# Optimization experiments

Hardware: AMD Instinct MI355X
Metric: run time of the kernel (lower is better)

## Reference

```python
import jax, jax.numpy as jnp
import numpy as np

DIM = 1024
FF = 4096
E = 8
K = 2


def setup_inputs() -> dict:
    key = jax.random.key(0)
    ks = jax.random.split(key, 6)
    x = jax.random.normal(ks[0], (4, 2048, DIM), dtype=jnp.float32)
    wr = jax.random.normal(ks[1], (E, DIM), dtype=jnp.float32) * 0.02   # router weight [E, D]
    w1 = jax.random.normal(ks[2], (E, DIM, 2 * FF), dtype=jnp.float32) * 0.02  # SwiGLU in-proj
    b1 = jax.random.normal(ks[3], (E, 2 * FF), dtype=jnp.float32) * 0.02
    w2 = jax.random.normal(ks[4], (E, FF, DIM), dtype=jnp.float32) * 0.02  # SwiGLU out-proj
    b2 = jax.random.normal(ks[5], (E, DIM), dtype=jnp.float32) * 0.02
    return {"x": x, "wr": wr, "w1": w1, "b1": b1, "w2": w2, "b2": b2}


def reference(x, wr, w1, b1, w2, b2):
    B, T, D = x.shape
    n_experts = wr.shape[0]
    xf = x.reshape(B * T, D)                      # [N, D]
    logits = xf @ wr.T                            # [N, E]
    topk_vals, topk_idx = jax.lax.top_k(logits, K)  # [N, K]
    gates = jax.nn.softmax(topk_vals, axis=-1)      # [N, K]
    out = jnp.zeros_like(xf)
    for e in range(n_experts):
        # combined gate weight for tokens routed to expert e (0 otherwise)
        g_e = jnp.sum(jnp.where(topk_idx == e, gates, 0.0), axis=-1)  # [N]
        u = xf @ w1[e] + b1[e]                    # [N, 2F]
        a, b = jnp.split(u, 2, axis=-1)
        h = jax.nn.silu(a) * b                    # SwiGLU
        y_e = h @ w2[e] + b2[e]                   # [N, D]
        out = out + g_e[:, None] * y_e
    return out.reshape(B, T, D)
```

## Files before the change

kernel.cpp:

```cpp
#include <hip/hip_runtime.h>

#define NE 8
#define NTOK 8192
#define NDIM 1024
#define NFF 4096

typedef short bf16x8 __attribute__((ext_vector_type(8)));
typedef float f32x4 __attribute__((ext_vector_type(4)));
typedef unsigned short us_t;
typedef us_t us4 __attribute__((ext_vector_type(4)));

#define MFMA16 __builtin_amdgcn_mfma_f32_16x16x32_bf16

__device__ __forceinline__ us_t f2bf(float f) {
  unsigned int u = __float_as_uint(f);
  u += 0x7fffu + ((u >> 16) & 1u);
  return (us_t)(u >> 16);
}

__device__ __forceinline__ void gload16(const void* g, void* l) {
  __builtin_amdgcn_global_load_lds(
      (const __attribute__((address_space(1))) void*)g,
      (__attribute__((address_space(3))) void*)l, 16, 0, 0);
}

__global__ __launch_bounds__(256) void router_kernel(
    const float* __restrict__ x, const float* __restrict__ wr,
    int* __restrict__ counts, int* __restrict__ tok_list,
    int4* __restrict__ tok4, float2* __restrict__ gate2,
    us_t* __restrict__ xbf)
{
  __shared__ float wr_s[NE * NDIM];
  int tid = threadIdx.x;
#pragma unroll
  for (int i = 0; i < 8; ++i)
    ((float4*)wr_s)[tid + 256 * i] = ((const float4*)wr)[tid + 256 * i];
  __syncthreads();
  int w = tid >> 6, l = tid & 63;
  int t = blockIdx.x * 4 + w;
  float4 xv[4];
#pragma unroll
  for (int j = 0; j < 4; ++j) xv[j] = ((const float4*)x)[(size_t)t * 256 + j * 64 + l];
#pragma unroll
  for (int j = 0; j < 4; ++j) {
    us4 o;
    o.x = f2bf(xv[j].x); o.y = f2bf(xv[j].y); o.z = f2bf(xv[j].z); o.w = f2bf(xv[j].w);
    ((us4*)xbf)[(size_t)t * 256 + j * 64 + l] = o;
  }
  float logits[NE];
#pragma unroll
  for (int e = 0; e < NE; ++e) {
    float p = 0.f;
#pragma unroll
    for (int j = 0; j < 4; ++j) {
      float4 wv = ((const float4*)wr_s)[e * 256 + j * 64 + l];
      p += xv[j].x * wv.x + xv[j].y * wv.y + xv[j].z * wv.z + xv[j].w * wv.w;
    }
#pragma unroll
    for (int s = 32; s > 0; s >>= 1) p += __shfl_xor(p, s, 64);
    logits[e] = p;
  }
  if (l == 0) {
    int e1 = 0; float v1 = logits[0];
#pragma unroll
    for (int e = 1; e < NE; ++e) if (logits[e] > v1) { v1 = logits[e]; e1 = e; }
    int e2 = -1; float v2 = -3.4e38f;
#pragma unroll
    for (int e = 0; e < NE; ++e) if (e != e1 && logits[e] > v2) { v2 = logits[e]; e2 = e; }
    float ge = expf(v2 - v1);
    float g1 = 1.f / (1.f + ge);
    float g2 = 1.f - g1;
    int i1 = atomicAdd(&counts[e1], 1);
    tok_list[e1 * NTOK + i1] = t;
    int i2 = atomicAdd(&counts[e2], 1);
    tok_list[e2 * NTOK + i2] = t;
    tok4[t] = make_int4(e1, i1, e2, i2);
    gate2[t] = make_float2(g1, g2);
  }
}

__global__ void prefix8(const int* __restrict__ counts, int* __restrict__ offsets) {
  if (threadIdx.x == 0) {
    int s = 0;
    for (int e = 0; e < NE; ++e) { offsets[e] = s; s += counts[e]; }
  }
}

__global__ __launch_bounds__(256) void transpose_cvt(
    const float* __restrict__ in, us_t* __restrict__ out, int R, int C)
{
  __shared__ float tile[64][65];
  int e = blockIdx.z;
  const float* ip = in + (size_t)e * R * C;
  us_t* op = out + (size_t)e * R * C;
  int r0 = blockIdx.y * 64, c0 = blockIdx.x * 64;
  int tid = threadIdx.x;
#pragma unroll
  for (int q = 0; q < 4; ++q) {
    int id = tid + 256 * q;
    int rr = id >> 4, c4 = id & 15;
    float4 v = *(const float4*)&ip[(size_t)(r0 + rr) * C + c0 + c4 * 4];
    tile[rr][c4 * 4 + 0] = v.x; tile[rr][c4 * 4 + 1] = v.y;
    tile[rr][c4 * 4 + 2] = v.z; tile[rr][c4 * 4 + 3] = v.w;
  }
  __syncthreads();
#pragma unroll
  for (int q = 0; q < 4; ++q) {
    int id = tid + 256 * q;
    int cc = id >> 4, r4 = id & 15;
    us4 o;
    o.x = f2bf(tile[r4 * 4 + 0][cc]);
    o.y = f2bf(tile[r4 * 4 + 1][cc]);
    o.z = f2bf(tile[r4 * 4 + 2][cc]);
    o.w = f2bf(tile[r4 * 4 + 3][cc]);
    *(us4*)&op[(size_t)(c0 + cc) * R + r0 + r4 * 4] = o;
  }
}

__global__ __launch_bounds__(256) void gemm1_swiglu(
    const us_t* __restrict__ xbf,
    const us_t* __restrict__ w1T,
    const float* __restrict__ b1,
    const int* __restrict__ counts, const int* __restrict__ offsets,
    const int* __restrict__ tok_list,
    us_t* __restrict__ hbuf)
{
  const int e = blockIdx.z, mt = blockIdx.y, ct = blockIdx.x;
  const int cnt = counts[e];
  if (mt * 128 >= cnt) return;
  const int off = offsets[e];
  const int tid = threadIdx.x, w = tid >> 6, l = tid & 63;
  const int wr_ = w >> 1, wc = w & 1;

  __shared__ char ldsA[16384];
  __shared__ char ldsB[32768];
  __shared__ int tok_l[128];

  if (tid < 128) {
    int r = mt * 128 + tid;
    tok_l[tid] = tok_list[e * NTOK + (r < cnt ? r : cnt - 1)];
  }
  __syncthreads();

  f32x4 zf = {0.f, 0.f, 0.f, 0.f};
  f32x4 acc[2][4][4];
#pragma unroll
  for (int h_ = 0; h_ < 2; ++h_)
#pragma unroll
    for (int cg = 0; cg < 4; ++cg)
#pragma unroll
      for (int rg = 0; rg < 4; ++rg) acc[h_][cg][rg] = zf;

  const size_t w1base = (size_t)e * 2 * NFF * NDIM;

  for (int kt = 0; kt < NDIM; kt += 64) {
    __syncthreads();
#pragma unroll
    for (int i = 0; i < 12; ++i) {
      int c = w + i * 4;
      const us_t* gsrc; char* ldst;
      if (c < 16) {
        int p = c * 1024 + l * 16;
        int row = p >> 7;
        int ir = (p & 127) ^ ((row & 7) << 4);
        gsrc = xbf + (size_t)tok_l[row] * NDIM + kt + (ir >> 1);
        ldst = ldsA + c * 1024;
      } else {
        int cb = c - 16;
        int p = cb * 1024 + l * 16;
        int row = p >> 7;
        int ir = (p & 127) ^ ((row & 7) << 4);
        int ncol = (row < 128) ? (ct * 128 + row) : (NFF + ct * 128 + row - 128);
        gsrc = w1T + w1base + (size_t)ncol * NDIM + kt + (ir >> 1);
        ldst = ldsB + cb * 1024;
      }
      gload16(gsrc, ldst);
    }
    __syncthreads();
#pragma unroll
    for (int ks = 0; ks < 2; ++ks) {
      bf16x8 af[4];
#pragma unroll
      for (int rg = 0; rg < 4; ++rg) {
        int row = wr_ * 64 + rg * 16 + (l & 15);
        int ir = (ks * 64 + (l >> 4) * 16) ^ ((row & 7) << 4);
        af[rg] = *(const bf16x8*)(ldsA + row * 128 + ir);
      }
#pragma unroll
      for (int h_ = 0; h_ < 2; ++h_)
#pragma unroll
        for (int cg = 0; cg < 4; ++cg) {
          int crow = h_ * 128 + wc * 64 + cg * 16 + (l & 15);
          int ir = (ks * 64 + (l >> 4) * 16) ^ ((crow & 7) << 4);
          bf16x8 bfr = *(const bf16x8*)(ldsB + crow * 128 + ir);
#pragma unroll
          for (int rg = 0; rg < 4; ++rg)
            acc[h_][cg][rg] = MFMA16(af[rg], bfr, acc[h_][cg][rg], 0, 0, 0);
        }
    }
  }

  float b1a[4], b1b[4];
#pragma unroll
  for (int cg = 0; cg < 4; ++cg) {
    int n_a = ct * 128 + wc * 64 + cg * 16 + (l & 15);
    b1a[cg] = b1[e * 2 * NFF + n_a];
    b1b[cg] = b1[e * 2 * NFF + NFF + n_a];
  }
#pragma unroll
  for (int cg = 0; cg < 4; ++cg) {
    int n_a = ct * 128 + wc * 64 + cg * 16 + (l & 15);
#pragma unroll
    for (int rg = 0; rg < 4; ++rg) {
#pragma unroll
      for (int j = 0; j < 4; ++j) {
        int rt = wr_ * 64 + rg * 16 + (l >> 4) * 4 + j;
        int r = mt * 128 + rt;
        if (r < cnt) {
          float a = acc[0][cg][rg][j] + b1a[cg];
          float b = acc[1][cg][rg][j] + b1b[cg];
          float hv = (a / (1.f + __expf(-a))) * b;
          hbuf[(size_t)(off + r) * NFF + n_a] = f2bf(hv);
        }
      }
    }
  }
}

__global__ __launch_bounds__(256) void gemm2_slot(
    const us_t* __restrict__ hbuf,
    const us_t* __restrict__ w2T,
    const float* __restrict__ b2,
    const int* __restrict__ counts, const int* __restrict__ offsets,
    float* __restrict__ ybuf)
{
  const int e = blockIdx.z, mt = blockIdx.y, nt = blockIdx.x;
  const int cnt = counts[e];
  if (mt * 128 >= cnt) return;
  const int off = offsets[e];
  const int tid = threadIdx.x, w = tid >> 6, l = tid & 63;
  const int wr_ = w >> 1, wc = w & 1;

  __shared__ char ldsA[16384];
  __shared__ char ldsB[32768];

  f32x4 zf = {0.f, 0.f, 0.f, 0.f};
  f32x4 acc[2][4][4];
#pragma unroll
  for (int h_ = 0; h_ < 2; ++h_)
#pragma unroll
    for (int cg = 0; cg < 4; ++cg)
#pragma unroll
      for (int rg = 0; rg < 4; ++rg) acc[h_][cg][rg] = zf;

  const size_t w2base = (size_t)e * NDIM * NFF;

  for (int kt = 0; kt < NFF; kt += 64) {
    __syncthreads();
#pragma unroll
    for (int i = 0; i < 12; ++i) {
      int c = w + i * 4;
      const us_t* gsrc; char* ldst;
      if (c < 16) {
        int p = c * 1024 + l * 16;
        int row = p >> 7;
        int ir = (p & 127) ^ ((row & 7) << 4);
        int r = mt * 128 + row; if (r >= cnt) r = cnt - 1;
        gsrc = hbuf + (size_t)(off + r) * NFF + kt + (ir >> 1);
        ldst = ldsA + c * 1024;
      } else {
        int cb = c - 16;
        int p = cb * 1024 + l * 16;
        int row = p >> 7;
        int ir = (p & 127) ^ ((row & 7) << 4);
        int ncol = nt * 256 + row;
        gsrc = w2T + w2base + (size_t)ncol * NFF + kt + (ir >> 1);
        ldst = ldsB + cb * 1024;
      }
      gload16(gsrc, ldst);
    }
    __syncthreads();
#pragma unroll
    for (int ks = 0; ks < 2; ++ks) {
      bf16x8 af[4];
#pragma unroll
      for (int rg = 0; rg < 4; ++rg) {
        int row = wr_ * 64 + rg * 16 + (l & 15);
        int ir = (ks * 64 + (l >> 4) * 16) ^ ((row & 7) << 4);
        af[rg] = *(const bf16x8*)(ldsA + row * 128 + ir);
      }
#pragma unroll
      for (int h_ = 0; h_ < 2; ++h_)
#pragma unroll
        for (int cg = 0; cg < 4; ++cg) {
          int crow = h_ * 128 + wc * 64 + cg * 16 + (l & 15);
          int ir = (ks * 64 + (l >> 4) * 16) ^ ((crow & 7) << 4);
          bf16x8 bfr = *(const bf16x8*)(ldsB + crow * 128 + ir);
#pragma unroll
          for (int rg = 0; rg < 4; ++rg)
            acc[h_][cg][rg] = MFMA16(af[rg], bfr, acc[h_][cg][rg], 0, 0, 0);
        }
    }
  }

#pragma unroll
  for (int h_ = 0; h_ < 2; ++h_)
#pragma unroll
    for (int cg = 0; cg < 4; ++cg) {
      int col = nt * 256 + h_ * 128 + wc * 64 + cg * 16 + (l & 15);
      float b2v = b2[e * NDIM + col];
#pragma unroll
      for (int rg = 0; rg < 4; ++rg) {
#pragma unroll
        for (int j = 0; j < 4; ++j) {
          int rt = wr_ * 64 + rg * 16 + (l >> 4) * 4 + j;
          int r = mt * 128 + rt;
          if (r < cnt)
            ybuf[(size_t)(off + r) * NDIM + col] = acc[h_][cg][rg][j] + b2v;
        }
      }
    }
}

__global__ __launch_bounds__(256) void combine_kernel(
    const float* __restrict__ ybuf, const int* __restrict__ offsets,
    const int4* __restrict__ tok4, const float2* __restrict__ gate2,
    float* __restrict__ out)
{
  int t = blockIdx.x;
  int4 p = tok4[t];
  float2 g = gate2[t];
  int s1 = offsets[p.x] + p.y;
  int s2 = offsets[p.z] + p.w;
  const float4* y1 = (const float4*)(ybuf + (size_t)s1 * NDIM);
  const float4* y2 = (const float4*)(ybuf + (size_t)s2 * NDIM);
  float4 a = y1[threadIdx.x];
  float4 b = y2[threadIdx.x];
  float4 o;
  o.x = g.x * a.x + g.y * b.x;
  o.y = g.x * a.y + g.y * b.y;
  o.z = g.x * a.z + g.y * b.z;
  o.w = g.x * a.w + g.y * b.w;
  ((float4*)(out + (size_t)t * NDIM))[threadIdx.x] = o;
}

extern "C" void kernel_launch(void* const* d_in, const int* in_sizes, int n_in,
                              void* d_out, int out_size, void* d_ws, size_t ws_size,
                              hipStream_t stream) {
  const float* x  = (const float*)d_in[0];
  const float* wr = (const float*)d_in[1];
  const float* w1 = (const float*)d_in[2];
  const float* b1 = (const float*)d_in[3];
  const float* w2 = (const float*)d_in[4];
  const float* b2 = (const float*)d_in[5];
  float* out = (float*)d_out;
  char* ws = (char*)d_ws;

  int*    counts   = (int*)(ws + 0);
  int*    offsets  = (int*)(ws + 256);
  int*    tok_list = (int*)(ws + 512);
  int4*   tok4     = (int4*)(ws + 512 + 262144);
  float2* gate2    = (float2*)(ws + 512 + 262144 + 131072);
  us_t*   xbf      = (us_t*)(ws + 524800);
  us_t*   hbuf     = (us_t*)(ws + 524800 + (size_t)NTOK * NDIM * 2);
  us_t*   wT       = (us_t*)(ws + 524800 + (size_t)NTOK * NDIM * 2
                                          + (size_t)2 * NTOK * NFF * 2);
  float*  ybuf     = (float*)((char*)wT + 67108864);

  hipMemsetAsync(counts, 0, 32, stream);

  router_kernel<<<NTOK / 4, 256, 0, stream>>>(x, wr, counts, tok_list, tok4, gate2, xbf);
  prefix8<<<1, 64, 0, stream>>>(counts, offsets);

  transpose_cvt<<<dim3(2 * NFF / 64, NDIM / 64, NE), 256, 0, stream>>>(w1, wT, NDIM, 2 * NFF);
  gemm1_swiglu<<<dim3(NFF / 128, NTOK / 128, NE), 256, 0, stream>>>(
      xbf, wT, b1, counts, offsets, tok_list, hbuf);

  transpose_cvt<<<dim3(NDIM / 64, NFF / 64, NE), 256, 0, stream>>>(w2, wT, NFF, NDIM);
  gemm2_slot<<<dim3(NDIM / 256, NTOK / 128, NE), 256, 0, stream>>>(
      hbuf, wT, b2, counts, offsets, ybuf);

  combine_kernel<<<NTOK, 256, 0, stream>>>(ybuf, offsets, tok4, gate2, out);
}
```

Baseline: 1.075 ms.

## Remap gemm2 grid for XCD-local weight reuse and widen transpose stores

Flattens the gemm2 launch into a 1D grid and decodes block IDs so that all M-tiles sharing the same expert and N-tile land on the same XCD (block index mod 8). The aim is better L2 reuse of the w2 tiles. Row slot indices for the A tile are precomputed once into shared memory instead of being clamped inside the K loop. The transpose-convert kernel now writes 8 bf16 values per store instead of 4, which halves the number of store instructions. The mapping relies on the driver's round-robin assignment of blocks to XCDs.

```diff
diff --git a/kernel.cpp b/kernel.cpp
--- a/kernel.cpp
+++ b/kernel.cpp
@@ -9,6 +9,7 @@
 typedef float f32x4 __attribute__((ext_vector_type(4)));
 typedef unsigned short us_t;
 typedef us_t us4 __attribute__((ext_vector_type(4)));
+typedef us_t us8 __attribute__((ext_vector_type(8)));
 
 #define MFMA16 __builtin_amdgcn_mfma_f32_16x16x32_bf16
 
@@ -105,15 +106,13 @@
   }
   __syncthreads();
 #pragma unroll
-  for (int q = 0; q < 4; ++q) {
+  for (int q = 0; q < 2; ++q) {
     int id = tid + 256 * q;
-    int cc = id >> 4, r4 = id & 15;
-    us4 o;
-    o.x = f2bf(tile[r4 * 4 + 0][cc]);
-    o.y = f2bf(tile[r4 * 4 + 1][cc]);
-    o.z = f2bf(tile[r4 * 4 + 2][cc]);
-    o.w = f2bf(tile[r4 * 4 + 3][cc]);
-    *(us4*)&op[(size_t)(c0 + cc) * R + r0 + r4 * 4] = o;
+    int cc = id >> 3, r8 = id & 7;
+    us8 o;
+#pragma unroll
+    for (int j = 0; j < 8; ++j) o[j] = f2bf(tile[r8 * 8 + j][cc]);
+    *(us8*)&op[(size_t)(c0 + cc) * R + r0 + r8 * 8] = o;
   }
 }
 
@@ -234,7 +233,12 @@
     const int* __restrict__ counts, const int* __restrict__ offsets,
     float* __restrict__ ybuf)
 {
-  const int e = blockIdx.z, mt = blockIdx.y, nt = blockIdx.x;
+  const int b = blockIdx.x;
+  const int xcd = b & 7, k = b >> 3;
+  const int mt = k & 63;
+  const int combo = xcd + 8 * (k >> 6);
+  const int nt = combo & 3, e = combo >> 2;
+
   const int cnt = counts[e];
   if (mt * 128 >= cnt) return;
   const int off = offsets[e];
@@ -243,6 +247,13 @@
 
   __shared__ char ldsA[16384];
   __shared__ char ldsB[32768];
+  __shared__ int slot_l[128];
+
+  if (tid < 128) {
+    int r = mt * 128 + tid;
+    slot_l[tid] = off + (r < cnt ? r : cnt - 1);
+  }
+  __syncthreads();
 
   f32x4 zf = {0.f, 0.f, 0.f, 0.f};
   f32x4 acc[2][4][4];
@@ -265,8 +276,7 @@
         int p = c * 1024 + l * 16;
         int row = p >> 7;
         int ir = (p & 127) ^ ((row & 7) << 4);
-        int r = mt * 128 + row; if (r >= cnt) r = cnt - 1;
-        gsrc = hbuf + (size_t)(off + r) * NFF + kt + (ir >> 1);
+        gsrc = hbuf + (size_t)slot_l[row] * NFF + kt + (ir >> 1);
         ldst = ldsA + c * 1024;
       } else {
         int cb = c - 16;
@@ -377,7 +387,7 @@
       xbf, wT, b1, counts, offsets, tok_list, hbuf);
 
   transpose_cvt<<<dim3(NDIM / 64, NFF / 64, NE), 256, 0, stream>>>(w2, wT, NFF, NDIM);
-  gemm2_slot<<<dim3(NDIM / 256, NTOK / 128, NE), 256, 0, stream>>>(
+  gemm2_slot<<<2048, 256, 0, stream>>>(
       hbuf, wT, b2, counts, offsets, ybuf);
 
   combine_kernel<<<NTOK, 256, 0, stream>>>(ybuf, offsets, tok4, gate2, out);
```

New measurement: 1.091 ms. Within noise of the previous version (+1.5%).
